# Optimization experiments

Measured on AMD Instinct MI355X. Metric: run time of the kernel, lower is better.

The kernel has to match this reference:

```python
import jax, jax.numpy as jnp
import numpy as np

NUM_HEADS = 8
WINDOW = 7
DILATION = 1
EPS = 1e-5


def channel_ln(x, w, b):
    # x: [B, C, H, W]; normalize over channel dim (axis=1)
    mu = jnp.mean(x, axis=1, keepdims=True)
    var = jnp.var(x, axis=1, keepdims=True)
    xhat = (x - mu) * jax.lax.rsqrt(var + EPS)
    return xhat * w[None, :, None, None] + b[None, :, None, None]


def local_mask(H, W, window, dilation):
    r = (window // 2) * dilation
    ii, jj = jnp.meshgrid(jnp.arange(H), jnp.arange(W), indexing="ij")
    ii = ii.reshape(-1)
    jj = jj.reshape(-1)
    di = jnp.abs(ii[:, None] - ii[None, :])
    dj = jnp.abs(jj[:, None] - jj[None, :])
    m = (di <= r) & (dj <= r)
    if dilation > 1:
        m = m & (di % dilation == 0) & (dj % dilation == 0)
    return m  # [N, N] bool


def local_attention(x, qkv_w, qkv_b, proj_w, proj_b):
    B, C, H, W = x.shape
    N = H * W
    hd = C // NUM_HEADS
    t = x.reshape(B, C, N).transpose(0, 2, 1)            # [B, N, C]
    qkv = t @ qkv_w.T + qkv_b                            # [B, N, 3C]
    qkv = qkv.reshape(B, N, 3, NUM_HEADS, hd)
    q, k, v = (qkv[:, :, i].transpose(0, 2, 1, 3) for i in range(3))  # [B,h,N,d]
    scale = 1.0 / jnp.sqrt(jnp.asarray(hd, x.dtype))
    scores = jnp.einsum("bhnd,bhmd->bhnm", q, k) * scale  # [B,h,N,N]
    mask = local_mask(H, W, WINDOW, DILATION)             # [N,N]
    scores = jnp.where(mask[None, None], scores, jnp.asarray(-jnp.inf, x.dtype))
    attn = jax.nn.softmax(scores, axis=-1)
    out = jnp.einsum("bhnm,bhmd->bhnd", attn, v)          # [B,h,N,d]
    out = out.transpose(0, 2, 1, 3).reshape(B, N, C)      # [B,N,C]
    out = out @ proj_w.T + proj_b
    return out.transpose(0, 2, 1).reshape(B, C, H, W)


def mlp2d(x, fc1_w, fc1_b, fc2_w, fc2_b):
    # 1x1 convs == per-pixel linear over channels
    h = jnp.einsum("bchw,oc->bohw", x, fc1_w) + fc1_b[None, :, None, None]
    h = jax.nn.gelu(h, approximate=False)
    return jnp.einsum("bchw,oc->bohw", h, fc2_w) + fc2_b[None, :, None, None]


def setup_inputs() -> dict:
    key = jax.random.key(0)
    ks = jax.random.split(key, 12)
    B, C, H, W = 1, 256, 56, 56
    hidden = 4 * C
    s = lambda fan: 1.0 / np.sqrt(fan)
    return {
        "x": jax.random.normal(ks[0], (B, C, H, W), jnp.float32),
        "norm1_w": jnp.ones((C,), jnp.float32),
        "norm1_b": jnp.zeros((C,), jnp.float32),
        "qkv_w": jax.random.normal(ks[1], (3 * C, C), jnp.float32) * s(C),
        "qkv_b": jnp.zeros((3 * C,), jnp.float32),
        "proj_w": jax.random.normal(ks[2], (C, C), jnp.float32) * s(C),
        "proj_b": jnp.zeros((C,), jnp.float32),
        "norm2_w": jnp.ones((C,), jnp.float32),
        "norm2_b": jnp.zeros((C,), jnp.float32),
        "fc1_w": jax.random.normal(ks[3], (hidden, C), jnp.float32) * s(C),
        "fc1_b": jnp.zeros((hidden,), jnp.float32),
        "fc2_w": jax.random.normal(ks[4], (C, hidden), jnp.float32) * s(hidden),
        "fc2_b": jnp.zeros((C,), jnp.float32),
    }


def reference(x, norm1_w, norm1_b, qkv_w, qkv_b, proj_w, proj_b,
              norm2_w, norm2_b, fc1_w, fc1_b, fc2_w, fc2_b):
    x = x + local_attention(channel_ln(x, norm1_w, norm1_b), qkv_w, qkv_b, proj_w, proj_b)
    x = x + mlp2d(channel_ln(x, norm2_w, norm2_b), fc1_w, fc1_b, fc2_w, fc2_b)
    return x
```

## Files before the change

### kernel.cpp

```cpp
#include <hip/hip_runtime.h>
#include <math.h>


typedef unsigned int uint;
typedef unsigned short ushort;
typedef unsigned long long u64;
typedef __attribute__((ext_vector_type(8))) short short8;
typedef __attribute__((ext_vector_type(4))) float floatx4;
typedef __attribute__((ext_vector_type(4))) unsigned short ushort4v;

#define AS1(p) (const __attribute__((address_space(1))) void*)(p)
#define AS3(p) (__attribute__((address_space(3))) void*)(p)

__device__ __forceinline__ float bf2f(ushort u) {
  union { uint i; float f; } v; v.i = ((uint)u) << 16; return v.f;
}
__device__ __forceinline__ ushort f2bf(float f) {
  union { float f; uint i; } v; v.f = f;
  uint u = v.i;
  return (ushort)((u + 0x7fffu + ((u >> 16) & 1u)) >> 16);
}

__device__ __forceinline__ void stage64(const ushort* src, int kstride,
                                        ushort* dstBase, int tid) {
  const int srow = tid >> 5;
  const int scb  = (tid & 31) ^ srow;
  const ushort* g = src + (size_t)srow * kstride + scb * 8;
  ushort* d = dstBase + tid * 8;
  #pragma unroll
  for (int r = 0; r < 8; ++r) {
    __builtin_amdgcn_global_load_lds(AS1(g), AS3(d), 16, 0, 0);
    g += 8 * kstride;
    d += 2048;
  }
}

__device__ __forceinline__ void compute64(const ushort* As, const ushort* Bs,
                                          int w, int lane, floatx4 acc[4]) {
  const int fm = lane & 15;
  const int q  = lane >> 4;
  const int swz = fm & 7;
  const int arow = (w * 16 + fm) * 256;
  #pragma unroll
  for (int kt = 0; kt < 8; ++kt) {
    const int blk = ((kt * 4 + q) ^ swz) * 8;
    short8 af = *(const short8*)&As[arow + blk];
    #pragma unroll
    for (int nt = 0; nt < 4; ++nt) {
      short8 bfr = *(const short8*)&Bs[(nt * 16 + fm) * 256 + blk];
      acc[nt] = __builtin_amdgcn_mfma_f32_16x16x32_bf16(af, bfr, acc[nt], 0, 0, 0);
    }
  }
}

__global__ __launch_bounds__(256) void prep_kernel(
    const float* __restrict__ x, const float* __restrict__ n1w,
    const float* __restrict__ n1b,
    const float* __restrict__ qkvw, const float* __restrict__ projw,
    const float* __restrict__ f1w, const float* __restrict__ f2w,
    float* __restrict__ xT, ushort* __restrict__ t1, ushort* __restrict__ wcat)
{
  const int tid = threadIdx.x;
  const int bid = blockIdx.x;
  if (bid >= 196) {
    int idx = (bid - 196) * 256 + tid;
    float v;
    if (idx < 196608)       v = qkvw[idx];
    else if (idx < 262144)  v = projw[idx - 196608];
    else if (idx < 524288)  v = f1w[idx - 262144];
    else                    v = f2w[idx - 524288];
    wcat[idx] = f2bf(v);
    return;
  }
  __shared__ float tile[256 * 17];
  __shared__ float red[2][16][16];
  __shared__ float mu[16], rsv[16];
  const int n0 = bid * 16;
  const int px = tid & 15, grp = tid >> 4;
  #pragma unroll 4
  for (int it = 0; it < 16; ++it) {
    int c = it * 16 + grp;
    tile[c * 17 + px] = x[(size_t)c * 3136 + n0 + px];
  }
  __syncthreads();
  float s = 0.f, ss = 0.f;
  #pragma unroll
  for (int i = 0; i < 16; ++i) {
    float v = tile[(grp * 16 + i) * 17 + px];
    s += v; ss += v * v;
  }
  red[0][px][grp] = s; red[1][px][grp] = ss;
  __syncthreads();
  if (tid < 16) {
    float s2 = 0.f, ss2 = 0.f;
    #pragma unroll
    for (int g = 0; g < 16; ++g) { s2 += red[0][tid][g]; ss2 += red[1][tid][g]; }
    float m = s2 * (1.f / 256.f);
    float var = ss2 * (1.f / 256.f) - m * m;
    mu[tid] = m;
    rsv[tid] = rsqrtf(var + 1e-5f);
  }
  __syncthreads();
  const float wc = n1w[tid], bc = n1b[tid];
  #pragma unroll 4
  for (int p = 0; p < 16; ++p) {
    float v = tile[tid * 17 + p];
    xT[(size_t)(n0 + p) * 256 + tid] = v;
    t1[(size_t)(n0 + p) * 256 + tid] = f2bf((v - mu[p]) * rsv[p] * wc + bc);
  }
}

__global__ __launch_bounds__(256, 2) void qkv_kernel(
    const ushort* __restrict__ A, const ushort* __restrict__ B,
    const float* __restrict__ bias, ushort* __restrict__ out)
{
  __shared__ ushort As[16384], Bs[16384];
  const int tid = threadIdx.x, lane = tid & 63, w = tid >> 6;
  const int m0 = blockIdx.y * 64, n0 = blockIdx.x * 64;
  floatx4 acc[4] = {{0.f,0.f,0.f,0.f},{0.f,0.f,0.f,0.f},
                    {0.f,0.f,0.f,0.f},{0.f,0.f,0.f,0.f}};
  stage64(A + (size_t)m0 * 256, 256, As, tid);
  stage64(B + (size_t)n0 * 256, 256, Bs, tid);
  asm volatile("s_waitcnt vmcnt(0)" ::: "memory");
  __syncthreads();
  compute64(As, Bs, w, lane, acc);
  const int fm = lane & 15, q4 = (lane >> 4) * 4;
  #pragma unroll
  for (int nt = 0; nt < 4; ++nt)
    #pragma unroll
    for (int r = 0; r < 4; ++r) {
      int m = m0 + w * 16 + q4 + r;
      int n = n0 + nt * 16 + fm;
      float v = acc[nt][r] + bias[n];
      if (n < 256) v *= 0.17677669529663687f;
      out[(size_t)m * 768 + n] = f2bf(v);
    }
}

#define ATTN_SMEM 144416

__global__ __launch_bounds__(256, 1) void attnproj_kernel(
    const ushort* __restrict__ qkv, const ushort* __restrict__ pw_bf,
    const float* __restrict__ projb, const float* __restrict__ xT,
    float* __restrict__ x1)
{
  __shared__ __align__(16) char smem[ATTN_SMEM];
  ushort* Kh  = (ushort*)smem;
  ushort* Vh  = (ushort*)(smem + 52000);
  float*  pr  = (float*)(smem + 103200);
  ushort* aas = (ushort*)(smem + 135968);
  ushort* Bs0 = (ushort*)smem;
  ushort* Bs1 = (ushort*)(smem + 103200);

  const int tid = threadIdx.x;
  const int i0 = (blockIdx.x / 14) * 4, j0 = (blockIdx.x % 14) * 4;

  for (int s = tid; s < 3200; s += 256) {
    int p = s >> 5, ck = s & 31;
    int ii = i0 - 3 + p / 10, jj = j0 - 3 + p % 10;
    if (ii >= 0 && ii < 56 && jj >= 0 && jj < 56) {
      const ushort* kr = qkv + (size_t)(ii * 56 + jj) * 768 + 256 + ck * 8;
      short8 kv = *(const short8*)kr;
      u64 lo = ((const u64*)&kv)[0], hi = ((const u64*)&kv)[1];
      *(u64*)&Kh[p * 260 + ck * 8] = lo;
      *(u64*)&Kh[p * 260 + ck * 8 + 4] = hi;
      *(short8*)&Vh[p * 256 + ck * 8] = *(const short8*)(kr + 256);
    } else {
      *(u64*)&Kh[p * 260 + ck * 8] = 0ull;
      *(u64*)&Kh[p * 260 + ck * 8 + 4] = 0ull;
      short8 z = {0, 0, 0, 0, 0, 0, 0, 0};
      *(short8*)&Vh[p * 256 + ck * 8] = z;
    }
  }
  __syncthreads();

  const int wv = tid >> 6, lane = tid & 63;
  const int h = lane >> 3, mg = lane & 7;
  for (int qq = 0; qq < 4; ++qq) {
    const int p = wv * 4 + qq;
    const int qi = p >> 2, qj = p & 3;
    const int iq = i0 + qi, jq = j0 + qj;
    const ushort* qp = qkv + (size_t)(iq * 56 + jq) * 768 + h * 32;
    float qf[32];
    #pragma unroll
    for (int u = 0; u < 4; ++u) {
      short8 qv = *(const short8*)(qp + u * 8);
      #pragma unroll
      for (int e = 0; e < 8; ++e) qf[u * 8 + e] = bf2f((ushort)qv[e]);
    }
    float sv[7];
    float mx = -1e30f;
    #pragma unroll
    for (int k = 0; k < 7; ++k) {
      int m = mg + 8 * k;
      float s = -1e30f;
      if (m < 49) {
        int mi = m / 7, mj = m % 7;
        int ii = iq + mi - 3, jj = jq + mj - 3;
        if (ii >= 0 && ii < 56 && jj >= 0 && jj < 56) {
          int hrow = (qi + mi) * 10 + (qj + mj);
          const u64* k8 = (const u64*)&Kh[hrow * 260 + h * 32];
          float a = 0.f;
          #pragma unroll
          for (int u = 0; u < 8; ++u) {
            u64 kv = k8[u];
            #pragma unroll
            for (int e = 0; e < 4; ++e)
              a += qf[u * 4 + e] * bf2f((ushort)(kv >> (16 * e)));
          }
          s = a;
        }
      }
      sv[k] = s;
      mx = fmaxf(mx, s);
    }
    mx = fmaxf(mx, __shfl_xor(mx, 1));
    mx = fmaxf(mx, __shfl_xor(mx, 2));
    mx = fmaxf(mx, __shfl_xor(mx, 4));
    float sm = 0.f;
    #pragma unroll
    for (int k = 0; k < 7; ++k) { sv[k] = __expf(sv[k] - mx); sm += sv[k]; }
    sm += __shfl_xor(sm, 1);
    sm += __shfl_xor(sm, 2);
    sm += __shfl_xor(sm, 4);
    float inv = 1.f / sm;
    #pragma unroll
    for (int k = 0; k < 7; ++k) {
      int m = mg + 8 * k;
      pr[(p * 8 + h) * 64 + m] = sv[k] * inv;
    }
  }
  __syncthreads();

  stage64(pw_bf, 256, Bs0, tid);

  {
    const int qsel = tid >> 5, cg = tid & 31, hh = cg >> 2;
    #pragma unroll
    for (int pass = 0; pass < 2; ++pass) {
      const int p = pass * 8 + qsel;
      const int qi = p >> 2, qj = p & 3;
      float acc8[8] = {0, 0, 0, 0, 0, 0, 0, 0};
      #pragma unroll
      for (int mi = 0; mi < 7; ++mi)
        #pragma unroll
        for (int mj = 0; mj < 7; ++mj) {
          int m = mi * 7 + mj;
          int hrow = (qi + mi) * 10 + (qj + mj);
          float pm = pr[(p * 8 + hh) * 64 + m];
          short8 v8 = *(const short8*)&Vh[hrow * 256 + cg * 8];
          #pragma unroll
          for (int e = 0; e < 8; ++e)
            acc8[e] += pm * bf2f((ushort)v8[e]);
        }
      short8 o;
      #pragma unroll
      for (int e = 0; e < 8; ++e) o[e] = (short)f2bf(acc8[e]);
      *(short8*)&aas[p * 264 + cg * 8] = o;
    }
  }
  __syncthreads();

  const int fm = lane & 15, q = lane >> 4, q4 = q * 4;
  for (int c = 0; c < 4; ++c) {
    if (c > 0) __syncthreads();
    if (c < 3) {
      stage64(pw_bf + (size_t)(c + 1) * 64 * 256, 256, (c & 1) ? Bs0 : Bs1, tid);
      asm volatile("s_waitcnt vmcnt(8)" ::: "memory");
    } else {
      asm volatile("s_waitcnt vmcnt(0)" ::: "memory");
    }
    __syncthreads();
    const ushort* Bc = (c & 1) ? Bs1 : Bs0;
    floatx4 acc = {0.f, 0.f, 0.f, 0.f};
    const int rr = wv * 16 + fm;
    #pragma unroll
    for (int kt = 0; kt < 8; ++kt) {
      short8 af = *(const short8*)&aas[fm * 264 + kt * 32 + q * 8];
      short8 bfr = *(const short8*)&Bc[rr * 256 + (((kt * 4 + q) ^ (fm & 7))) * 8];
      acc = __builtin_amdgcn_mfma_f32_16x16x32_bf16(af, bfr, acc, 0, 0, 0);
    }
    const int ch = c * 64 + wv * 16 + fm;
    #pragma unroll
    for (int r = 0; r < 4; ++r) {
      int p = q4 + r;
      int n = (i0 + (p >> 2)) * 56 + j0 + (p & 3);
      x1[(size_t)n * 256 + ch] = acc[r] + projb[ch] + xT[(size_t)n * 256 + ch];
    }
  }
}

__global__ __launch_bounds__(256, 2) void mlp_kernel(
    const float* __restrict__ x1, const ushort* __restrict__ f1_bf,
    const float* __restrict__ f1b, const ushort* __restrict__ f2_bf,
    const float* __restrict__ f2b, const float* __restrict__ n2w,
    const float* __restrict__ n2b, float* __restrict__ outf)
{
  __shared__ ushort t2s[16 * 256];
  __shared__ ushort hbuf[16 * 1024];
  __shared__ ushort slab[4][2][2048];
  __shared__ float pstat[4][16][2];
  __shared__ float stats[16][2];

  const int tid = threadIdx.x;
  const int n0 = blockIdx.x * 16;
  const int w = tid >> 6;
  const int lane = tid & 63;
  const int fm = lane & 15;
  const int px = tid & 15;
  const int q = (lane >> 4) & 3;
  const int l4 = lane >> 2, lb = lane & 3;

  floatx4 xv[4];
  #pragma unroll
  for (int mc = 0; mc < 4; ++mc)
    xv[mc] = *(const floatx4*)(x1 + (size_t)(n0 + px) * 256 + w * 64 + mc * 16 + q * 4);
  float s = 0.f, ss = 0.f;
  #pragma unroll
  for (int mc = 0; mc < 4; ++mc)
    #pragma unroll
    for (int e = 0; e < 4; ++e) { s += xv[mc][e]; ss += xv[mc][e] * xv[mc][e]; }
  s += __shfl_xor(s, 16); ss += __shfl_xor(ss, 16);
  s += __shfl_xor(s, 32); ss += __shfl_xor(ss, 32);
  if (lane < 16) { pstat[w][px][0] = s; pstat[w][px][1] = ss; }
  __syncthreads();
  if (tid < 16) {
    float s2 = 0.f, ss2 = 0.f;
    #pragma unroll
    for (int ww = 0; ww < 4; ++ww) { s2 += pstat[ww][tid][0]; ss2 += pstat[ww][tid][1]; }
    float mu = s2 * (1.f / 256.f);
    float var = ss2 * (1.f / 256.f) - mu * mu;
    stats[tid][0] = mu;
    stats[tid][1] = rsqrtf(var + 1e-5f);
  }
  __syncthreads();
  {
    float mu = stats[px][0], rs = stats[px][1];
    #pragma unroll
    for (int mc = 0; mc < 4; ++mc) {
      int ch0 = w * 64 + mc * 16 + q * 4;
      ushort4v o;
      #pragma unroll
      for (int e = 0; e < 4; ++e)
        o[e] = f2bf((xv[mc][e] - mu) * rs * n2w[ch0 + e] + n2b[ch0 + e]);
      int slot = (ch0 >> 3) ^ (px & 7);
      *(ushort4v*)&t2s[px * 256 + slot * 8 + (ch0 & 7)] = o;
    }
  }
  float f1br[4][4];
  #pragma unroll
  for (int ci = 0; ci < 4; ++ci)
    #pragma unroll
    for (int nt = 0; nt < 4; ++nt)
      f1br[ci][nt] = f1b[(ci * 4 + w) * 64 + nt * 16 + fm];
  __syncthreads();

  ushort* sb0 = slab[w][0];
  ushort* sb1 = slab[w][1];

  {
    #define STAGE_F1(nc, kt, buf) do { \
      _Pragma("unroll") \
      for (int i_ = 0; i_ < 4; ++i_) { \
        int row_ = i_ * 16 + l4; \
        const ushort* g_ = f1_bf + (size_t)((nc) * 64 + row_) * 256 + (kt) * 32 + (lb ^ (row_ & 3)) * 8; \
        __builtin_amdgcn_global_load_lds(AS1(g_), AS3((buf) + i_ * 512 + lane * 8), 16, 0, 0); \
      } } while (0)

    floatx4 fa[4] = {{0.f,0.f,0.f,0.f},{0.f,0.f,0.f,0.f},
                     {0.f,0.f,0.f,0.f},{0.f,0.f,0.f,0.f}};
    STAGE_F1(w, 0, sb0);
    for (int sidx = 0; sidx < 32; ++sidx) {
      const int kt = sidx & 7;
      const int nc = (sidx >> 3) * 4 + w;
      ushort* cur = (sidx & 1) ? sb1 : sb0;
      ushort* nxt = (sidx & 1) ? sb0 : sb1;
      if (sidx < 31) {
        int s1 = sidx + 1;
        STAGE_F1((s1 >> 3) * 4 + w, s1 & 7, nxt);
        asm volatile("s_waitcnt vmcnt(4)" ::: "memory");
      } else {
        asm volatile("s_waitcnt vmcnt(0)" ::: "memory");
      }
      short8 af = *(const short8*)&t2s[fm * 256 + (((kt * 4 + q) ^ (fm & 7)) * 8)];
      #pragma unroll
      for (int nt = 0; nt < 4; ++nt) {
        int r = nt * 16 + fm;
        short8 bfr = *(const short8*)&cur[r * 32 + (q ^ (r & 3)) * 8];
        fa[nt] = __builtin_amdgcn_mfma_f32_16x16x32_bf16(af, bfr, fa[nt], 0, 0, 0);
      }
      if (kt == 7) {
        #pragma unroll
        for (int nt = 0; nt < 4; ++nt) {
          int hc = nc * 64 + nt * 16 + fm;
          int hslotbase = (hc >> 3);
          #pragma unroll
          for (int r4 = 0; r4 < 4; ++r4) {
            int prow = q * 4 + r4;
            float v = fa[nt][r4] + f1br[sidx >> 3][nt];
            v = 0.5f * v * (1.0f + erff(v * 0.70710678118654752f));
            hbuf[prow * 1024 + ((hslotbase ^ (prow & 7)) * 8) + (hc & 7)] = f2bf(v);
            fa[nt][r4] = 0.f;
          }
        }
      }
    }
    #undef STAGE_F1
  }
  __syncthreads();

  {
    #define STAGE_F2(kt, buf) do { \
      _Pragma("unroll") \
      for (int i_ = 0; i_ < 4; ++i_) { \
        int row_ = i_ * 16 + l4; \
        const ushort* g_ = f2_bf + (size_t)(w * 64 + row_) * 1024 + (kt) * 32 + (lb ^ (row_ & 3)) * 8; \
        __builtin_amdgcn_global_load_lds(AS1(g_), AS3((buf) + i_ * 512 + lane * 8), 16, 0, 0); \
      } } while (0)

    floatx4 ga[4] = {{0.f,0.f,0.f,0.f},{0.f,0.f,0.f,0.f},
                     {0.f,0.f,0.f,0.f},{0.f,0.f,0.f,0.f}};
    STAGE_F2(0, sb0);
    for (int kt = 0; kt < 32; ++kt) {
      ushort* cur = (kt & 1) ? sb1 : sb0;
      ushort* nxt = (kt & 1) ? sb0 : sb1;
      if (kt < 31) {
        STAGE_F2(kt + 1, nxt);
        asm volatile("s_waitcnt vmcnt(4)" ::: "memory");
      } else {
        asm volatile("s_waitcnt vmcnt(0)" ::: "memory");
      }
      short8 bfr = *(const short8*)&hbuf[fm * 1024 + (((kt * 4 + q) ^ (fm & 7)) * 8)];
      #pragma unroll
      for (int mt = 0; mt < 4; ++mt) {
        int r = mt * 16 + fm;
        short8 af = *(const short8*)&cur[r * 32 + (q ^ (r & 3)) * 8];
        ga[mt] = __builtin_amdgcn_mfma_f32_16x16x32_bf16(af, bfr, ga[mt], 0, 0, 0);
      }
    }
    #undef STAGE_F2
    #pragma unroll
    for (int mt = 0; mt < 4; ++mt) {
      #pragma unroll
      for (int r4 = 0; r4 < 4; ++r4) {
        int ch = w * 64 + mt * 16 + q * 4 + r4;
        float v = ga[mt][r4] + f2b[ch] + xv[mt][r4];
        outf[(size_t)ch * 3136 + n0 + fm] = v;
      }
    }
  }
}

extern "C" void kernel_launch(void* const* d_in, const int* in_sizes, int n_in,
                              void* d_out, int out_size, void* d_ws, size_t ws_size,
                              hipStream_t stream) {
  const float* x     = (const float*)d_in[0];
  const float* n1w   = (const float*)d_in[1];
  const float* n1b   = (const float*)d_in[2];
  const float* qkvw  = (const float*)d_in[3];
  const float* qkvb  = (const float*)d_in[4];
  const float* projw = (const float*)d_in[5];
  const float* projb = (const float*)d_in[6];
  const float* n2w   = (const float*)d_in[7];
  const float* n2b   = (const float*)d_in[8];
  const float* f1w   = (const float*)d_in[9];
  const float* f1b   = (const float*)d_in[10];
  const float* f2w   = (const float*)d_in[11];
  const float* f2b   = (const float*)d_in[12];

  char* ws = (char*)d_ws;
  ushort* wcat = (ushort*)(ws + 0);
  float*  xT   = (float*)(ws + 1572864);
  ushort* t    = (ushort*)(ws + 4784128);
  ushort* qh   = (ushort*)(ws + 6389760);
  float*  x1   = (float*)(ws + 12812288);

  const ushort* qw_bf = wcat;
  const ushort* pw_bf = wcat + 196608;
  const ushort* f1_bf = wcat + 262144;
  const ushort* f2_bf = wcat + 524288;
  float* outf = (float*)d_out;

  hipLaunchKernelGGL(prep_kernel, dim3(3268), dim3(256), 0, stream,
                     x, n1w, n1b, qkvw, projw, f1w, f2w, xT, t, wcat);
  hipLaunchKernelGGL(qkv_kernel, dim3(12, 49), dim3(256), 0, stream,
                     t, qw_bf, qkvb, qh);
  hipLaunchKernelGGL(attnproj_kernel, dim3(196), dim3(256), 0, stream,
                     qh, pw_bf, projb, xT, x1);
  hipLaunchKernelGGL(mlp_kernel, dim3(196), dim3(256), 0, stream,
                     x1, f1_bf, f1b, f2_bf, f2b, n2w, n2b, outf);
}
```

Before: 145.1 us.

## Fuse attention+proj and MLP into one 512-thread kernel with LDS handoff

Merges the attention/projection kernel and the MLP kernel into one kernel per 4x4 pixel tile, keeping the post-attention residual x1 in shared memory instead of writing and re-reading it from global memory. The block grows to 512 threads (8 waves), so each wave handles half as many query pixels, projection channels and MLP channels, with per-wave double-buffered weight staging via global_load_lds. This removes a kernel launch and an x1 global round trip, and raises wave count per block. In exchange it keeps 196 blocks at one block per CU with a large LDS footprint, and the MLP now runs on the spatial tile ordering.

```diff
diff --git a/kernel.cpp b/kernel.cpp
--- a/kernel.cpp
+++ b/kernel.cpp
@@ -137,25 +137,36 @@
     }
 }
 
-#define ATTN_SMEM 144416
-
-__global__ __launch_bounds__(256, 1) void attnproj_kernel(
+#define AM_SMEM 144448
+
+__global__ __launch_bounds__(512, 1) void attnmlp_kernel(
     const ushort* __restrict__ qkv, const ushort* __restrict__ pw_bf,
     const float* __restrict__ projb, const float* __restrict__ xT,
-    float* __restrict__ x1)
+    const ushort* __restrict__ f1_bf, const float* __restrict__ f1b,
+    const ushort* __restrict__ f2_bf, const float* __restrict__ f2b,
+    const float* __restrict__ n2w, const float* __restrict__ n2b,
+    float* __restrict__ outf)
 {
-  __shared__ __align__(16) char smem[ATTN_SMEM];
-  ushort* Kh  = (ushort*)smem;
-  ushort* Vh  = (ushort*)(smem + 52000);
-  float*  pr  = (float*)(smem + 103200);
-  ushort* aas = (ushort*)(smem + 135968);
-  ushort* Bs0 = (ushort*)smem;
-  ushort* Bs1 = (ushort*)(smem + 103200);
+  __shared__ __align__(16) char smem[AM_SMEM];
+  ushort* Kh    = (ushort*)smem;
+  ushort* Vh    = (ushort*)(smem + 52000);
+  float*  pr    = (float*)(smem + 103200);
+  ushort* aas   = (ushort*)(smem + 136000);
+  ushort* pslab = (ushort*)smem;
+  float*  x1s   = (float*)(smem + 103200);
+  ushort* hbuf  = (ushort*)smem;
+  ushort* fslab = (ushort*)(smem + 32768);
+  ushort* t2s   = (ushort*)(smem + 120096);
+  float*  pstat = (float*)(smem + 128288);
+  float*  stats = (float*)(smem + 129312);
 
   const int tid = threadIdx.x;
+  const int wv = tid >> 6, lane = tid & 63;
+  const int fm = lane & 15, q = lane >> 4;
+  const int l4 = lane >> 2, lb = lane & 3;
   const int i0 = (blockIdx.x / 14) * 4, j0 = (blockIdx.x % 14) * 4;
 
-  for (int s = tid; s < 3200; s += 256) {
+  for (int s = tid; s < 3200; s += 512) {
     int p = s >> 5, ck = s & 31;
     int ii = i0 - 3 + p / 10, jj = j0 - 3 + p % 10;
     if (ii >= 0 && ii < 56 && jj >= 0 && jj < 56) {
@@ -174,210 +185,201 @@
   }
   __syncthreads();
 
-  const int wv = tid >> 6, lane = tid & 63;
-  const int h = lane >> 3, mg = lane & 7;
-  for (int qq = 0; qq < 4; ++qq) {
-    const int p = wv * 4 + qq;
+  {
+    const int h = lane >> 3, mg = lane & 7;
+    #pragma unroll
+    for (int qq = 0; qq < 2; ++qq) {
+      const int p = wv * 2 + qq;
+      const int qi = p >> 2, qj = p & 3;
+      const int iq = i0 + qi, jq = j0 + qj;
+      const ushort* qp = qkv + (size_t)(iq * 56 + jq) * 768 + h * 32;
+      float qf[32];
+      #pragma unroll
+      for (int u = 0; u < 4; ++u) {
+        short8 qv = *(const short8*)(qp + u * 8);
+        #pragma unroll
+        for (int e = 0; e < 8; ++e) qf[u * 8 + e] = bf2f((ushort)qv[e]);
+      }
+      float sv[7];
+      float mx = -1e30f;
+      #pragma unroll
+      for (int k = 0; k < 7; ++k) {
+        int m = mg + 8 * k;
+        float s = -1e30f;
+        if (m < 49) {
+          int mi = m / 7, mj = m % 7;
+          int ii = iq + mi - 3, jj = jq + mj - 3;
+          if (ii >= 0 && ii < 56 && jj >= 0 && jj < 56) {
+            int hrow = (qi + mi) * 10 + (qj + mj);
+            const u64* k8 = (const u64*)&Kh[hrow * 260 + h * 32];
+            float a = 0.f;
+            #pragma unroll
+            for (int u = 0; u < 8; ++u) {
+              u64 kv = k8[u];
+              #pragma unroll
+              for (int e = 0; e < 4; ++e)
+                a += qf[u * 4 + e] * bf2f((ushort)(kv >> (16 * e)));
+            }
+            s = a;
+          }
+        }
+        sv[k] = s;
+        mx = fmaxf(mx, s);
+      }
+      mx = fmaxf(mx, __shfl_xor(mx, 1));
+      mx = fmaxf(mx, __shfl_xor(mx, 2));
+      mx = fmaxf(mx, __shfl_xor(mx, 4));
+      float sm = 0.f;
+      #pragma unroll
+      for (int k = 0; k < 7; ++k) { sv[k] = __expf(sv[k] - mx); sm += sv[k]; }
+      sm += __shfl_xor(sm, 1);
+      sm += __shfl_xor(sm, 2);
+      sm += __shfl_xor(sm, 4);
+      float inv = 1.f / sm;
+      #pragma unroll
+      for (int k = 0; k < 7; ++k) {
+        int m = mg + 8 * k;
+        pr[(p * 8 + h) * 64 + m] = sv[k] * inv;
+      }
+    }
+  }
+  __syncthreads();
+
+  ushort* ps0 = pslab + wv * 2048;
+  ushort* ps1 = ps0 + 1024;
+#define STAGE_P(kt, buf) do { \
+    _Pragma("unroll") \
+    for (int i_ = 0; i_ < 2; ++i_) { \
+      int row_ = i_ * 16 + l4; \
+      const ushort* g_ = pw_bf + (size_t)(wv * 32 + row_) * 256 + (kt) * 32 + (lb ^ (row_ & 3)) * 8; \
+      __builtin_amdgcn_global_load_lds(AS1(g_), AS3((buf) + i_ * 512 + lane * 8), 16, 0, 0); \
+    } } while (0)
+  STAGE_P(0, ps0);
+
+  {
+    const int p = tid >> 5, cg = tid & 31, hh = cg >> 2;
     const int qi = p >> 2, qj = p & 3;
-    const int iq = i0 + qi, jq = j0 + qj;
-    const ushort* qp = qkv + (size_t)(iq * 56 + jq) * 768 + h * 32;
-    float qf[32];
-    #pragma unroll
-    for (int u = 0; u < 4; ++u) {
-      short8 qv = *(const short8*)(qp + u * 8);
-      #pragma unroll
-      for (int e = 0; e < 8; ++e) qf[u * 8 + e] = bf2f((ushort)qv[e]);
-    }
-    float sv[7];
-    float mx = -1e30f;
-    #pragma unroll
-    for (int k = 0; k < 7; ++k) {
-      int m = mg + 8 * k;
-      float s = -1e30f;
-      if (m < 49) {
-        int mi = m / 7, mj = m % 7;
-        int ii = iq + mi - 3, jj = jq + mj - 3;
-        if (ii >= 0 && ii < 56 && jj >= 0 && jj < 56) {
-          int hrow = (qi + mi) * 10 + (qj + mj);
-          const u64* k8 = (const u64*)&Kh[hrow * 260 + h * 32];
-          float a = 0.f;
-          #pragma unroll
-          for (int u = 0; u < 8; ++u) {
-            u64 kv = k8[u];
-            #pragma unroll
-            for (int e = 0; e < 4; ++e)
-              a += qf[u * 4 + e] * bf2f((ushort)(kv >> (16 * e)));
-          }
-          s = a;
-        }
-      }
-      sv[k] = s;
-      mx = fmaxf(mx, s);
-    }
-    mx = fmaxf(mx, __shfl_xor(mx, 1));
-    mx = fmaxf(mx, __shfl_xor(mx, 2));
-    mx = fmaxf(mx, __shfl_xor(mx, 4));
-    float sm = 0.f;
-    #pragma unroll
-    for (int k = 0; k < 7; ++k) { sv[k] = __expf(sv[k] - mx); sm += sv[k]; }
-    sm += __shfl_xor(sm, 1);
-    sm += __shfl_xor(sm, 2);
-    sm += __shfl_xor(sm, 4);
-    float inv = 1.f / sm;
-    #pragma unroll
-    for (int k = 0; k < 7; ++k) {
-      int m = mg + 8 * k;
-      pr[(p * 8 + h) * 64 + m] = sv[k] * inv;
-    }
-  }
-  __syncthreads();
-
-  stage64(pw_bf, 256, Bs0, tid);
-
-  {
-    const int qsel = tid >> 5, cg = tid & 31, hh = cg >> 2;
-    #pragma unroll
-    for (int pass = 0; pass < 2; ++pass) {
-      const int p = pass * 8 + qsel;
-      const int qi = p >> 2, qj = p & 3;
-      float acc8[8] = {0, 0, 0, 0, 0, 0, 0, 0};
-      #pragma unroll
-      for (int mi = 0; mi < 7; ++mi)
+    float acc8[8] = {0, 0, 0, 0, 0, 0, 0, 0};
+    #pragma unroll
+    for (int mi = 0; mi < 7; ++mi)
+      #pragma unroll
+      for (int mj = 0; mj < 7; ++mj) {
+        int m = mi * 7 + mj;
+        int hrow = (qi + mi) * 10 + (qj + mj);
+        float pm = pr[(p * 8 + hh) * 64 + m];
+        short8 v8 = *(const short8*)&Vh[hrow * 256 + cg * 8];
         #pragma unroll
-        for (int mj = 0; mj < 7; ++mj) {
-          int m = mi * 7 + mj;
-          int hrow = (qi + mi) * 10 + (qj + mj);
-          float pm = pr[(p * 8 + hh) * 64 + m];
-          short8 v8 = *(const short8*)&Vh[hrow * 256 + cg * 8];
-          #pragma unroll
-          for (int e = 0; e < 8; ++e)
-            acc8[e] += pm * bf2f((ushort)v8[e]);
-        }
-      short8 o;
-      #pragma unroll
-      for (int e = 0; e < 8; ++e) o[e] = (short)f2bf(acc8[e]);
-      *(short8*)&aas[p * 264 + cg * 8] = o;
-    }
-  }
-  __syncthreads();
-
-  const int fm = lane & 15, q = lane >> 4, q4 = q * 4;
-  for (int c = 0; c < 4; ++c) {
-    if (c > 0) __syncthreads();
-    if (c < 3) {
-      stage64(pw_bf + (size_t)(c + 1) * 64 * 256, 256, (c & 1) ? Bs0 : Bs1, tid);
-      asm volatile("s_waitcnt vmcnt(8)" ::: "memory");
-    } else {
-      asm volatile("s_waitcnt vmcnt(0)" ::: "memory");
-    }
-    __syncthreads();
-    const ushort* Bc = (c & 1) ? Bs1 : Bs0;
-    floatx4 acc = {0.f, 0.f, 0.f, 0.f};
-    const int rr = wv * 16 + fm;
-    #pragma unroll
+        for (int e = 0; e < 8; ++e)
+          acc8[e] += pm * bf2f((ushort)v8[e]);
+      }
+    short8 o;
+    #pragma unroll
+    for (int e = 0; e < 8; ++e) o[e] = (short)f2bf(acc8[e]);
+    *(short8*)&aas[p * 264 + cg * 8] = o;
+  }
+  __syncthreads();
+
+  {
+    floatx4 pacc[2] = {{0.f,0.f,0.f,0.f},{0.f,0.f,0.f,0.f}};
     for (int kt = 0; kt < 8; ++kt) {
+      ushort* cur = (kt & 1) ? ps1 : ps0;
+      ushort* nxt = (kt & 1) ? ps0 : ps1;
+      if (kt < 7) {
+        STAGE_P(kt + 1, nxt);
+        asm volatile("s_waitcnt vmcnt(2)" ::: "memory");
+      } else {
+        asm volatile("s_waitcnt vmcnt(0)" ::: "memory");
+      }
       short8 af = *(const short8*)&aas[fm * 264 + kt * 32 + q * 8];
-      short8 bfr = *(const short8*)&Bc[rr * 256 + (((kt * 4 + q) ^ (fm & 7))) * 8];
-      acc = __builtin_amdgcn_mfma_f32_16x16x32_bf16(af, bfr, acc, 0, 0, 0);
-    }
-    const int ch = c * 64 + wv * 16 + fm;
-    #pragma unroll
-    for (int r = 0; r < 4; ++r) {
-      int p = q4 + r;
-      int n = (i0 + (p >> 2)) * 56 + j0 + (p & 3);
-      x1[(size_t)n * 256 + ch] = acc[r] + projb[ch] + xT[(size_t)n * 256 + ch];
-    }
-  }
-}
-
-__global__ __launch_bounds__(256, 2) void mlp_kernel(
-    const float* __restrict__ x1, const ushort* __restrict__ f1_bf,
-    const float* __restrict__ f1b, const ushort* __restrict__ f2_bf,
-    const float* __restrict__ f2b, const float* __restrict__ n2w,
-    const float* __restrict__ n2b, float* __restrict__ outf)
-{
-  __shared__ ushort t2s[16 * 256];
-  __shared__ ushort hbuf[16 * 1024];
-  __shared__ ushort slab[4][2][2048];
-  __shared__ float pstat[4][16][2];
-  __shared__ float stats[16][2];
-
-  const int tid = threadIdx.x;
-  const int n0 = blockIdx.x * 16;
-  const int w = tid >> 6;
-  const int lane = tid & 63;
-  const int fm = lane & 15;
-  const int px = tid & 15;
-  const int q = (lane >> 4) & 3;
-  const int l4 = lane >> 2, lb = lane & 3;
-
-  floatx4 xv[4];
-  #pragma unroll
-  for (int mc = 0; mc < 4; ++mc)
-    xv[mc] = *(const floatx4*)(x1 + (size_t)(n0 + px) * 256 + w * 64 + mc * 16 + q * 4);
-  float s = 0.f, ss = 0.f;
-  #pragma unroll
-  for (int mc = 0; mc < 4; ++mc)
-    #pragma unroll
-    for (int e = 0; e < 4; ++e) { s += xv[mc][e]; ss += xv[mc][e] * xv[mc][e]; }
-  s += __shfl_xor(s, 16); ss += __shfl_xor(ss, 16);
-  s += __shfl_xor(s, 32); ss += __shfl_xor(ss, 32);
-  if (lane < 16) { pstat[w][px][0] = s; pstat[w][px][1] = ss; }
+      #pragma unroll
+      for (int nt = 0; nt < 2; ++nt) {
+        int r = nt * 16 + fm;
+        short8 bfr = *(const short8*)&cur[r * 32 + (q ^ (r & 3)) * 8];
+        pacc[nt] = __builtin_amdgcn_mfma_f32_16x16x32_bf16(af, bfr, pacc[nt], 0, 0, 0);
+      }
+    }
+    #pragma unroll
+    for (int nt = 0; nt < 2; ++nt) {
+      int ch = wv * 32 + nt * 16 + fm;
+      #pragma unroll
+      for (int r = 0; r < 4; ++r) {
+        int px = q * 4 + r;
+        int n = (i0 + (px >> 2)) * 56 + j0 + (px & 3);
+        x1s[px * 264 + ch] = pacc[nt][r] + projb[ch] + xT[(size_t)n * 256 + ch];
+      }
+    }
+  }
+  ushort* fs0 = fslab + wv * 4096;
+  ushort* fs1 = fs0 + 2048;
+#define STAGE_F1(c, kt, buf) do { \
+    _Pragma("unroll") \
+    for (int i_ = 0; i_ < 4; ++i_) { \
+      int row_ = i_ * 16 + l4; \
+      const ushort* g_ = f1_bf + (size_t)((c) * 64 + row_) * 256 + (kt) * 32 + (lb ^ (row_ & 3)) * 8; \
+      __builtin_amdgcn_global_load_lds(AS1(g_), AS3((buf) + i_ * 512 + lane * 8), 16, 0, 0); \
+    } } while (0)
+  STAGE_F1(wv, 0, fs0);
+  __syncthreads();
+
+  floatx4 xv[2];
+  xv[0] = *(const floatx4*)&x1s[fm * 264 + wv * 32 + q * 4];
+  xv[1] = *(const floatx4*)&x1s[fm * 264 + wv * 32 + 16 + q * 4];
+  {
+    float s = 0.f, ss = 0.f;
+    #pragma unroll
+    for (int nt = 0; nt < 2; ++nt)
+      #pragma unroll
+      for (int e = 0; e < 4; ++e) { s += xv[nt][e]; ss += xv[nt][e] * xv[nt][e]; }
+    s += __shfl_xor(s, 16); ss += __shfl_xor(ss, 16);
+    s += __shfl_xor(s, 32); ss += __shfl_xor(ss, 32);
+    if (lane < 16) { pstat[(wv * 16 + lane) * 2] = s; pstat[(wv * 16 + lane) * 2 + 1] = ss; }
+  }
   __syncthreads();
   if (tid < 16) {
     float s2 = 0.f, ss2 = 0.f;
     #pragma unroll
-    for (int ww = 0; ww < 4; ++ww) { s2 += pstat[ww][tid][0]; ss2 += pstat[ww][tid][1]; }
+    for (int ww = 0; ww < 8; ++ww) {
+      s2 += pstat[(ww * 16 + tid) * 2];
+      ss2 += pstat[(ww * 16 + tid) * 2 + 1];
+    }
     float mu = s2 * (1.f / 256.f);
     float var = ss2 * (1.f / 256.f) - mu * mu;
-    stats[tid][0] = mu;
-    stats[tid][1] = rsqrtf(var + 1e-5f);
-  }
-  __syncthreads();
-  {
-    float mu = stats[px][0], rs = stats[px][1];
-    #pragma unroll
-    for (int mc = 0; mc < 4; ++mc) {
-      int ch0 = w * 64 + mc * 16 + q * 4;
+    stats[tid * 2] = mu;
+    stats[tid * 2 + 1] = rsqrtf(var + 1e-5f);
+  }
+  __syncthreads();
+  {
+    float mu = stats[fm * 2], rs = stats[fm * 2 + 1];
+    #pragma unroll
+    for (int nt = 0; nt < 2; ++nt) {
+      int ch0 = wv * 32 + nt * 16 + q * 4;
       ushort4v o;
       #pragma unroll
       for (int e = 0; e < 4; ++e)
-        o[e] = f2bf((xv[mc][e] - mu) * rs * n2w[ch0 + e] + n2b[ch0 + e]);
-      int slot = (ch0 >> 3) ^ (px & 7);
-      *(ushort4v*)&t2s[px * 256 + slot * 8 + (ch0 & 7)] = o;
-    }
-  }
-  float f1br[4][4];
+        o[e] = f2bf((xv[nt][e] - mu) * rs * n2w[ch0 + e] + n2b[ch0 + e]);
+      int slot = ch0 >> 3;
+      *(ushort4v*)&t2s[fm * 256 + ((slot ^ (fm & 7)) * 8) + (ch0 & 7)] = o;
+    }
+  }
+  float f1br[2][4];
   #pragma unroll
-  for (int ci = 0; ci < 4; ++ci)
+  for (int ci = 0; ci < 2; ++ci)
     #pragma unroll
     for (int nt = 0; nt < 4; ++nt)
-      f1br[ci][nt] = f1b[(ci * 4 + w) * 64 + nt * 16 + fm];
-  __syncthreads();
-
-  ushort* sb0 = slab[w][0];
-  ushort* sb1 = slab[w][1];
-
-  {
-    #define STAGE_F1(nc, kt, buf) do { \
-      _Pragma("unroll") \
-      for (int i_ = 0; i_ < 4; ++i_) { \
-        int row_ = i_ * 16 + l4; \
-        const ushort* g_ = f1_bf + (size_t)((nc) * 64 + row_) * 256 + (kt) * 32 + (lb ^ (row_ & 3)) * 8; \
-        __builtin_amdgcn_global_load_lds(AS1(g_), AS3((buf) + i_ * 512 + lane * 8), 16, 0, 0); \
-      } } while (0)
-
+      f1br[ci][nt] = f1b[(wv + ci * 8) * 64 + nt * 16 + fm];
+  __syncthreads();
+
+  {
     floatx4 fa[4] = {{0.f,0.f,0.f,0.f},{0.f,0.f,0.f,0.f},
                      {0.f,0.f,0.f,0.f},{0.f,0.f,0.f,0.f}};
-    STAGE_F1(w, 0, sb0);
-    for (int sidx = 0; sidx < 32; ++sidx) {
+    for (int sidx = 0; sidx < 16; ++sidx) {
       const int kt = sidx & 7;
-      const int nc = (sidx >> 3) * 4 + w;
-      ushort* cur = (sidx & 1) ? sb1 : sb0;
-      ushort* nxt = (sidx & 1) ? sb0 : sb1;
-      if (sidx < 31) {
+      const int ci = sidx >> 3;
+      ushort* cur = (sidx & 1) ? fs1 : fs0;
+      ushort* nxt = (sidx & 1) ? fs0 : fs1;
+      if (sidx < 15) {
         int s1 = sidx + 1;
-        STAGE_F1((s1 >> 3) * 4 + w, s1 & 7, nxt);
+        STAGE_F1(wv + (s1 >> 3) * 8, s1 & 7, nxt);
         asm volatile("s_waitcnt vmcnt(4)" ::: "memory");
       } else {
         asm volatile("s_waitcnt vmcnt(0)" ::: "memory");
@@ -392,63 +394,63 @@
       if (kt == 7) {
         #pragma unroll
         for (int nt = 0; nt < 4; ++nt) {
-          int hc = nc * 64 + nt * 16 + fm;
-          int hslotbase = (hc >> 3);
+          int hc = (wv + ci * 8) * 64 + nt * 16 + fm;
           #pragma unroll
           for (int r4 = 0; r4 < 4; ++r4) {
             int prow = q * 4 + r4;
-            float v = fa[nt][r4] + f1br[sidx >> 3][nt];
+            float v = fa[nt][r4] + f1br[ci][nt];
             v = 0.5f * v * (1.0f + erff(v * 0.70710678118654752f));
-            hbuf[prow * 1024 + ((hslotbase ^ (prow & 7)) * 8) + (hc & 7)] = f2bf(v);
+            hbuf[prow * 1024 + (((hc >> 3) ^ (prow & 7)) * 8) + (hc & 7)] = f2bf(v);
             fa[nt][r4] = 0.f;
           }
         }
       }
     }
-    #undef STAGE_F1
-  }
-  __syncthreads();
-
-  {
-    #define STAGE_F2(kt, buf) do { \
-      _Pragma("unroll") \
-      for (int i_ = 0; i_ < 4; ++i_) { \
-        int row_ = i_ * 16 + l4; \
-        const ushort* g_ = f2_bf + (size_t)(w * 64 + row_) * 1024 + (kt) * 32 + (lb ^ (row_ & 3)) * 8; \
-        __builtin_amdgcn_global_load_lds(AS1(g_), AS3((buf) + i_ * 512 + lane * 8), 16, 0, 0); \
-      } } while (0)
-
-    floatx4 ga[4] = {{0.f,0.f,0.f,0.f},{0.f,0.f,0.f,0.f},
-                     {0.f,0.f,0.f,0.f},{0.f,0.f,0.f,0.f}};
-    STAGE_F2(0, sb0);
+  }
+  ushort* gs0 = fs0;
+  ushort* gs1 = fs0 + 1024;
+#define STAGE_F2(kt, buf) do { \
+    _Pragma("unroll") \
+    for (int i_ = 0; i_ < 2; ++i_) { \
+      int row_ = i_ * 16 + l4; \
+      const ushort* g_ = f2_bf + (size_t)(wv * 32 + row_) * 1024 + (kt) * 32 + (lb ^ (row_ & 3)) * 8; \
+      __builtin_amdgcn_global_load_lds(AS1(g_), AS3((buf) + i_ * 512 + lane * 8), 16, 0, 0); \
+    } } while (0)
+  STAGE_F2(0, gs0);
+  __syncthreads();
+
+  {
+    floatx4 ga[2] = {{0.f,0.f,0.f,0.f},{0.f,0.f,0.f,0.f}};
     for (int kt = 0; kt < 32; ++kt) {
-      ushort* cur = (kt & 1) ? sb1 : sb0;
-      ushort* nxt = (kt & 1) ? sb0 : sb1;
+      ushort* cur = (kt & 1) ? gs1 : gs0;
+      ushort* nxt = (kt & 1) ? gs0 : gs1;
       if (kt < 31) {
         STAGE_F2(kt + 1, nxt);
-        asm volatile("s_waitcnt vmcnt(4)" ::: "memory");
+        asm volatile("s_waitcnt vmcnt(2)" ::: "memory");
       } else {
         asm volatile("s_waitcnt vmcnt(0)" ::: "memory");
       }
       short8 bfr = *(const short8*)&hbuf[fm * 1024 + (((kt * 4 + q) ^ (fm & 7)) * 8)];
       #pragma unroll
-      for (int mt = 0; mt < 4; ++mt) {
+      for (int mt = 0; mt < 2; ++mt) {
         int r = mt * 16 + fm;
         short8 af = *(const short8*)&cur[r * 32 + (q ^ (r & 3)) * 8];
         ga[mt] = __builtin_amdgcn_mfma_f32_16x16x32_bf16(af, bfr, ga[mt], 0, 0, 0);
       }
     }
-    #undef STAGE_F2
-    #pragma unroll
-    for (int mt = 0; mt < 4; ++mt) {
+    #pragma unroll
+    for (int mt = 0; mt < 2; ++mt) {
       #pragma unroll
       for (int r4 = 0; r4 < 4; ++r4) {
-        int ch = w * 64 + mt * 16 + q * 4 + r4;
-        float v = ga[mt][r4] + f2b[ch] + xv[mt][r4];
-        outf[(size_t)ch * 3136 + n0 + fm] = v;
-      }
-    }
-  }
+        int ch = wv * 32 + mt * 16 + q * 4 + r4;
+        int n = (i0 + (fm >> 2)) * 56 + j0 + (fm & 3);
+        outf[(size_t)ch * 3136 + n] = ga[mt][r4] + f2b[ch] + xv[mt][r4];
+      }
+    }
+  }
+#undef STAGE_P
+#undef STAGE_F1
+#undef STAGE_F2
 }
 
 extern "C" void kernel_launch(void* const* d_in, const int* in_sizes, int n_in,
@@ -473,7 +475,6 @@
   float*  xT   = (float*)(ws + 1572864);
   ushort* t    = (ushort*)(ws + 4784128);
   ushort* qh   = (ushort*)(ws + 6389760);
-  float*  x1   = (float*)(ws + 12812288);
 
   const ushort* qw_bf = wcat;
   const ushort* pw_bf = wcat + 196608;
@@ -485,8 +486,7 @@
                      x, n1w, n1b, qkvw, projw, f1w, f2w, xT, t, wcat);
   hipLaunchKernelGGL(qkv_kernel, dim3(12, 49), dim3(256), 0, stream,
                      t, qw_bf, qkvb, qh);
-  hipLaunchKernelGGL(attnproj_kernel, dim3(196), dim3(256), 0, stream,
-                     qh, pw_bf, projb, xT, x1);
-  hipLaunchKernelGGL(mlp_kernel, dim3(196), dim3(256), 0, stream,
-                     x1, f1_bf, f1b, f2_bf, f2b, n2w, n2b, outf);
-}
+  hipLaunchKernelGGL(attnmlp_kernel, dim3(196), dim3(512), 0, stream,
+                     qh, pw_bf, projb, xT, f1_bf, f1b, f2_bf, f2b,
+                     n2w, n2b, outf);
+}
```

New measurement: 126.3 us. -13.0%, faster.
